# Kernel optimization log

Hardware: AMD Instinct MI355X
Metric: run time of the kernel (lower is better)

The kernel has to match this reference:

```python
import jax, jax.numpy as jnp
import numpy as np
from math import sqrt

N_HEADS = 4
IN_FEATURES = 64
KQ = 64
HEAD_V = IN_FEATURES // N_HEADS  # 16


def setup_inputs() -> dict:
    key = jax.random.key(0)
    ks = jax.random.split(key, 7)
    s = 0.05
    x = jax.random.normal(ks[0], (8192, IN_FEATURES), dtype=jnp.float32)
    # Per-head Linear weights stacked on a leading head axis.
    # torch Linear: y = x @ W.T + b; we store W already transposed: [H, F, E]
    Wq = jax.random.normal(ks[1], (N_HEADS, IN_FEATURES, KQ), dtype=jnp.float32) * s
    bq = jax.random.normal(ks[2], (N_HEADS, KQ), dtype=jnp.float32) * s
    Wk = jax.random.normal(ks[3], (N_HEADS, IN_FEATURES, KQ), dtype=jnp.float32) * s
    bk = jax.random.normal(ks[4], (N_HEADS, KQ), dtype=jnp.float32) * s
    Wv = jax.random.normal(ks[5], (N_HEADS, IN_FEATURES, HEAD_V), dtype=jnp.float32) * s
    bv = jax.random.normal(ks[6], (N_HEADS, HEAD_V), dtype=jnp.float32) * s
    return {"x": x, "Wq": Wq, "bq": bq, "Wk": Wk, "bk": bk, "Wv": Wv, "bv": bv}


def reference(x, Wq, bq, Wk, bk, Wv, bv):
    N, F = x.shape
    scale = 1.0 / sqrt(F)  # original divides by sqrt(in_features), NOT sqrt(kq)
    # Batched-head projections: [H, N, E]
    Q = jnp.einsum('nf,hfe->hne', x, Wq) + bq[:, None, :]
    K = jnp.einsum('nf,hfe->hne', x, Wk) + bk[:, None, :]
    V = jnp.einsum('nf,hfd->hnd', x, Wv) + bv[:, None, :]
    logits = jnp.einsum('hne,hme->hnm', Q, K) * scale  # [H, N, N]
    attn = jax.nn.softmax(logits, axis=-1)
    out_heads = jnp.einsum('hnm,hmd->hnd', attn, V)    # [H, N, HEAD_V]
    # Head i writes columns [i*HEAD_V:(i+1)*HEAD_V] of the output.
    out = jnp.transpose(out_heads, (1, 0, 2)).reshape(N, F)
    return out
```

## Files before the change

### kernel.cpp

```cpp
#include <hip/hip_runtime.h>

typedef __attribute__((ext_vector_type(4))) float f32x4;
typedef __attribute__((ext_vector_type(8))) short bf16x8;
typedef __attribute__((ext_vector_type(4))) short bf16x4;
typedef long fp8x8;

#define NH 4

static __device__ __forceinline__ unsigned short f2bf(float f){
  unsigned u = __float_as_uint(f);
  u += 0x7FFFu + ((u >> 16) & 1u);
  return (unsigned short)(u >> 16);
}

static __device__ __forceinline__ unsigned pack2bf(float a, float b){
  return __builtin_amdgcn_perm(__float_as_uint(b) + 0x8000u,
                               __float_as_uint(a) + 0x8000u, 0x07060302u);
}

static __device__ __forceinline__ unsigned pack2bf_t(float a, float b){
  return __builtin_amdgcn_perm(__float_as_uint(b), __float_as_uint(a), 0x07060302u);
}

static __device__ __forceinline__ int pack_fp8x4(float a, float b, float c, float d){
  int w = __builtin_amdgcn_cvt_pk_fp8_f32(a, b, 0, false);
  w     = __builtin_amdgcn_cvt_pk_fp8_f32(c, d, w, true);
  return w;
}

__global__ __launch_bounds__(256) void wprep_kernel(
    const float* __restrict__ Wq, const float* __restrict__ bq,
    const float* __restrict__ Wk, const float* __restrict__ bk,
    const float* __restrict__ Wv,
    unsigned short* __restrict__ WF, float* __restrict__ bias_s, int n)
{
  __shared__ unsigned short wqT[64*72];
  __shared__ unsigned short wkT[64*72];
  __shared__ unsigned short wvT[16*72];

  const int t = threadIdx.x;
  const int h = blockIdx.x;
  const float S1 = 0.4246609001f;
  const int f = t >> 2, eg = t & 3;

  {
    const float4* g = (const float4*)(Wq + h*4096 + f*64 + eg*16);
    #pragma unroll
    for (int p = 0; p < 4; ++p){
      float4 d = g[p];
      int e0 = eg*16 + p*4;
      wqT[(e0+0)*72 + f] = f2bf(d.x * S1);
      wqT[(e0+1)*72 + f] = f2bf(d.y * S1);
      wqT[(e0+2)*72 + f] = f2bf(d.z * S1);
      wqT[(e0+3)*72 + f] = f2bf(d.w * S1);
    }
  }
  {
    const float4* g = (const float4*)(Wk + h*4096 + f*64 + eg*16);
    #pragma unroll
    for (int p = 0; p < 4; ++p){
      float4 d = g[p];
      int e0 = eg*16 + p*4;
      wkT[(e0+0)*72 + f] = f2bf(d.x * S1);
      wkT[(e0+1)*72 + f] = f2bf(d.y * S1);
      wkT[(e0+2)*72 + f] = f2bf(d.z * S1);
      wkT[(e0+3)*72 + f] = f2bf(d.w * S1);
    }
  }
  {
    float4 d = *(const float4*)(Wv + h*1024 + f*16 + eg*4);
    int d0 = eg*4;
    wvT[(d0+0)*72 + f] = f2bf(d.x);
    wvT[(d0+1)*72 + f] = f2bf(d.y);
    wvT[(d0+2)*72 + f] = f2bf(d.z);
    wvT[(d0+3)*72 + f] = f2bf(d.w);
  }
  if (t < 64)       bias_s[h*128 + t] = bq[h*64 + t] * S1;
  else if (t < 128) bias_s[h*128 + t] = bk[h*64 + (t-64)] * S1;
  __syncthreads();

  const int lane = t & 63, w = t >> 6;
  const int quad = lane >> 4, l16 = lane & 15;
  for (int s = w; s < 18; s += 4){
    const unsigned short* src;
    if (s < 8){      int et = s>>1,     ks = s&1;     src = wqT + (et*16+l16)*72 + ks*32 + quad*8; }
    else if (s < 16){int ft = (s-8)>>1, ks = (s-8)&1; src = wkT + (ft*16+l16)*72 + ks*32 + quad*8; }
    else {           int ks = s-16;                   src = wvT + l16*72 + ks*32 + quad*8; }
    uint4 v = *(const uint4*)src;
    *(uint4*)(WF + ((size_t)(h*18 + s)*64 + lane)*8) = v;
  }
}

__global__ __launch_bounds__(256) void proj_kernel(
    const float* __restrict__ x, const float* __restrict__ bv,
    const unsigned short* __restrict__ WF, const float* __restrict__ bias_s,
    unsigned char* __restrict__ Qfr, unsigned char* __restrict__ Kt,
    unsigned short* __restrict__ Vt, int n)
{
  __shared__ unsigned short xf[8*64*8];
  __shared__ float bql[64], bkl[64], bvl[16];

  const int t  = threadIdx.x;
  const int h  = blockIdx.y;
  const int r0 = blockIdx.x * 64;

  {
    const int r = t >> 2, cg4 = t & 3;
    const float4* g = (const float4*)(x + (size_t)(r0 + r)*64 + cg4*16);
    float4 a = g[0], b = g[1], c = g[2], d = g[3];
    unsigned u0 = pack2bf(a.x,a.y), u1 = pack2bf(a.z,a.w);
    unsigned u2 = pack2bf(b.x,b.y), u3 = pack2bf(b.z,b.w);
    unsigned u4 = pack2bf(c.x,c.y), u5 = pack2bf(c.z,c.w);
    unsigned u6 = pack2bf(d.x,d.y), u7 = pack2bf(d.z,d.w);
    const int it = r >> 4, l16r = r & 15, ks = cg4 >> 1, q0 = (cg4 & 1)*2;
    uint4* dst0 = (uint4*)(xf + ((it*2+ks)*64 + q0*16     + l16r)*8);
    uint4* dst1 = (uint4*)(xf + ((it*2+ks)*64 + (q0+1)*16 + l16r)*8);
    *dst0 = make_uint4(u0,u1,u2,u3);
    *dst1 = make_uint4(u4,u5,u6,u7);
  }
  if (t < 64)        bql[t]     = bias_s[h*128 + t];
  else if (t < 128)  bkl[t-64]  = bias_s[h*128 + t];
  else if (t < 144)  bvl[t-128] = bv[h*16 + (t-128)];
  __syncthreads();

  const int lane = t & 63, w = t >> 6;
  const int quad = lane >> 4, l16 = lane & 15;

  bf16x8 xa[8];
  #pragma unroll
  for (int i = 0; i < 8; ++i)
    xa[i] = *(const bf16x8*)(xf + (i*64 + lane)*8);

  const unsigned short* WFh = WF + (size_t)h*18*64*8;
  bf16x8 wq0 = *(const bf16x8*)(WFh + ((size_t)(     w*2 + 0)*64 + lane)*8);
  bf16x8 wq1 = *(const bf16x8*)(WFh + ((size_t)(     w*2 + 1)*64 + lane)*8);
  bf16x8 wk0 = *(const bf16x8*)(WFh + ((size_t)(8  + w*2 + 0)*64 + lane)*8);
  bf16x8 wk1 = *(const bf16x8*)(WFh + ((size_t)(8  + w*2 + 1)*64 + lane)*8);
  bf16x8 wv0 = *(const bf16x8*)(WFh + ((size_t)16*64 + lane)*8);
  bf16x8 wv1 = *(const bf16x8*)(WFh + ((size_t)17*64 + lane)*8);

  const f32x4 z = {0.f,0.f,0.f,0.f};
  f32x4 accQ[4] = {z,z,z,z};
  f32x4 accK[4] = {z,z,z,z};
  f32x4 accV = z;

  #pragma unroll
  for (int it = 0; it < 4; ++it){
    accQ[it] = __builtin_amdgcn_mfma_f32_16x16x32_bf16(wq0, xa[it*2+0], accQ[it], 0,0,0);
    accQ[it] = __builtin_amdgcn_mfma_f32_16x16x32_bf16(wq1, xa[it*2+1], accQ[it], 0,0,0);
  }
  #pragma unroll
  for (int tt = 0; tt < 4; ++tt){
    accK[tt] = __builtin_amdgcn_mfma_f32_16x16x32_bf16(wk0, xa[tt*2+0], accK[tt], 0,0,0);
    accK[tt] = __builtin_amdgcn_mfma_f32_16x16x32_bf16(wk1, xa[tt*2+1], accK[tt], 0,0,0);
  }
  accV = __builtin_amdgcn_mfma_f32_16x16x32_bf16(xa[w*2+0], wv0, accV, 0,0,0);
  accV = __builtin_amdgcn_mfma_f32_16x16x32_bf16(xa[w*2+1], wv1, accV, 0,0,0);

  {
    const int e0 = w*16 + quad*4;
    const float b0 = bql[e0], b1 = bql[e0+1], b2 = bql[e0+2], b3 = bql[e0+3];
    const int qk = (e0 & 31) >> 3, hf = e0 >> 5, boff = (quad & 1) * 4;
    #pragma unroll
    for (int it = 0; it < 4; ++it){
      unsigned o = pack_fp8x4(accQ[it][0]+b0, accQ[it][1]+b1,
                              accQ[it][2]+b2, accQ[it][3]+b3);
      const int T = (r0 >> 4) + it;
      *(unsigned*)(Qfr + (size_t)h*((size_t)n<<6) + (size_t)T*1024
                       + (qk*16 + l16)*16 + hf*8 + boff) = o;
    }
  }
  {
    const int f0 = w*16 + quad*4;
    const float bk0 = bkl[f0], bk1 = bkl[f0+1], bk2 = bkl[f0+2], bk3 = bkl[f0+3];
    const int qk = (f0 & 31) >> 3, hf = f0 >> 5, boff = (quad & 1) * 4;
    #pragma unroll
    for (int tt = 0; tt < 4; ++tt){
      unsigned o = pack_fp8x4(accK[tt][0]+bk0, accK[tt][1]+bk1,
                              accK[tt][2]+bk2, accK[tt][3]+bk3);
      const int T = (r0 >> 4) + tt;
      *(unsigned*)(Kt + (size_t)h*((size_t)n<<6) + (size_t)T*1024
                      + (qk*16 + l16)*16 + hf*8 + boff) = o;
    }
  }
  {
    float bvv = bvl[l16];
    unsigned v01 = pack2bf(accV[0]+bvv, accV[1]+bvv);
    unsigned v23 = pack2bf(accV[2]+bvv, accV[3]+bvv);
    const int T = (r0 >> 4) + w;
    *(uint2*)(Vt + (size_t)h*((size_t)n<<4)
                 + ((size_t)(T>>1)*64 + lane)*8 + (T&1)*4) = make_uint2(v01, v23);
  }
}

__global__ __launch_bounds__(512, 4) void attn_kernel(
    const unsigned char* __restrict__ Qfr, const unsigned char* __restrict__ Kt,
    const unsigned short* __restrict__ Vt, float* __restrict__ out, int n)
{
  __shared__ float part[7][64][17];

  const int tid  = threadIdx.x;
  const int lane = tid & 63;
  const int jq   = tid >> 6;
  const int bid  = blockIdx.x;
  const int h    = bid & 3;
  const int iblk = bid >> 2;
  const int l16  = lane & 15, quad = lane >> 4;
  const int i0   = iblk*32;
  const int ntq  = (n >> 3) >> 4;
  const int nch  = ntq >> 1;
  const int tile0 = jq * ntq;

  const unsigned char* qfh = Qfr + (size_t)h*((size_t)n<<6);
  longlong2 q0 = *(const longlong2*)(qfh + (size_t)((i0>>4)    )*1024 + lane*16);
  longlong2 q1 = *(const longlong2*)(qfh + (size_t)((i0>>4) + 1)*1024 + lane*16);
  const fp8x8 qf00 = (fp8x8)q0.x;
  const fp8x8 qf01 = (fp8x8)q0.y;
  const fp8x8 qf10 = (fp8x8)q1.x;
  const fp8x8 qf11 = (fp8x8)q1.y;

  const longlong2* ktl = (const longlong2*)(Kt + (size_t)h*((size_t)n<<6)) + (size_t)tile0*64 + lane;
  const uint4*     vtu = (const uint4*)(Vt + (size_t)h*((size_t)n<<4)) + (size_t)(tile0>>1)*64 + lane;

  f32x4 o0  = {0.f,0.f,0.f,0.f};
  f32x4 o1  = {0.f,0.f,0.f,0.f};
  f32x4 la0 = {0.f,0.f,0.f,0.f};
  f32x4 la1 = {0.f,0.f,0.f,0.f};
  const f32x4 z = {0.f,0.f,0.f,0.f};
  const bf16x8 vones = {(short)0x3F80, (short)0x3F80, (short)0x3F80, (short)0x3F80,
                        (short)0x3F80, (short)0x3F80, (short)0x3F80, (short)0x3F80};

  longlong2 ka0 = ktl[0],   ka1 = ktl[64];
  uint4     va  = vtu[0];
  longlong2 kb0 = ktl[128], kb1 = ktl[192];
  uint4     vb  = vtu[64];

#define ATTN_CHUNK(KA, KB, VV)                                                \
  {                                                                           \
    fp8x8 a0 = (fp8x8)KA.x;                                                   \
    fp8x8 a1 = (fp8x8)KA.y;                                                   \
    fp8x8 b0 = (fp8x8)KB.x;                                                   \
    fp8x8 b1 = (fp8x8)KB.y;                                                   \
    f32x4 s0 = __builtin_amdgcn_mfma_f32_16x16x32_fp8_fp8(a0, qf00, z, 0,0,0);\
    s0 = __builtin_amdgcn_mfma_f32_16x16x32_fp8_fp8(a1, qf01, s0, 0,0,0);     \
    f32x4 s1 = __builtin_amdgcn_mfma_f32_16x16x32_fp8_fp8(a0, qf10, z, 0,0,0);\
    s1 = __builtin_amdgcn_mfma_f32_16x16x32_fp8_fp8(a1, qf11, s1, 0,0,0);     \
    f32x4 t0 = __builtin_amdgcn_mfma_f32_16x16x32_fp8_fp8(b0, qf00, z, 0,0,0);\
    t0 = __builtin_amdgcn_mfma_f32_16x16x32_fp8_fp8(b1, qf01, t0, 0,0,0);     \
    f32x4 t1 = __builtin_amdgcn_mfma_f32_16x16x32_fp8_fp8(b0, qf10, z, 0,0,0);\
    t1 = __builtin_amdgcn_mfma_f32_16x16x32_fp8_fp8(b1, qf11, t1, 0,0,0);     \
    float pa00 = __builtin_amdgcn_exp2f(s0[0]);                               \
    float pa01 = __builtin_amdgcn_exp2f(s0[1]);                               \
    float pa02 = __builtin_amdgcn_exp2f(s0[2]);                               \
    float pa03 = __builtin_amdgcn_exp2f(s0[3]);                               \
    float pa10 = __builtin_amdgcn_exp2f(s1[0]);                               \
    float pa11 = __builtin_amdgcn_exp2f(s1[1]);                               \
    float pa12 = __builtin_amdgcn_exp2f(s1[2]);                               \
    float pa13 = __builtin_amdgcn_exp2f(s1[3]);                               \
    float pb00 = __builtin_amdgcn_exp2f(t0[0]);                               \
    float pb01 = __builtin_amdgcn_exp2f(t0[1]);                               \
    float pb02 = __builtin_amdgcn_exp2f(t0[2]);                               \
    float pb03 = __builtin_amdgcn_exp2f(t0[3]);                               \
    float pb10 = __builtin_amdgcn_exp2f(t1[0]);                               \
    float pb11 = __builtin_amdgcn_exp2f(t1[1]);                               \
    float pb12 = __builtin_amdgcn_exp2f(t1[2]);                               \
    float pb13 = __builtin_amdgcn_exp2f(t1[3]);                               \
    union { uint4 u; bf16x8 v; } pq0, pq1, vfu;                               \
    pq0.u = make_uint4(pack2bf_t(pa00,pa01), pack2bf_t(pa02,pa03),            \
                       pack2bf_t(pb00,pb01), pack2bf_t(pb02,pb03));           \
    pq1.u = make_uint4(pack2bf_t(pa10,pa11), pack2bf_t(pa12,pa13),            \
                       pack2bf_t(pb10,pb11), pack2bf_t(pb12,pb13));           \
    vfu.u = VV;                                                               \
    o0  = __builtin_amdgcn_mfma_f32_16x16x32_bf16(pq0.v, vfu.v, o0,  0,0,0);  \
    o1  = __builtin_amdgcn_mfma_f32_16x16x32_bf16(pq1.v, vfu.v, o1,  0,0,0);  \
    la0 = __builtin_amdgcn_mfma_f32_16x16x32_bf16(pq0.v, vones, la0, 0,0,0);  \
    la1 = __builtin_amdgcn_mfma_f32_16x16x32_bf16(pq1.v, vones, la1, 0,0,0);  \
  }

  for (int c = 0; c < nch - 2; c += 2){
    ATTN_CHUNK(ka0, ka1, va)
    ka0 = ktl[256]; ka1 = ktl[320]; va = vtu[128];
    ATTN_CHUNK(kb0, kb1, vb)
    kb0 = ktl[384]; kb1 = ktl[448]; vb = vtu[192];
    ktl += 256; vtu += 128;
  }
  ATTN_CHUNK(ka0, ka1, va)
  ATTN_CHUNK(kb0, kb1, vb)
#undef ATTN_CHUNK

  if (jq > 0){
    float* p = &part[jq-1][lane][0];
    p[ 0]=o0[0];  p[ 1]=o0[1];  p[ 2]=o0[2];  p[ 3]=o0[3];
    p[ 4]=o1[0];  p[ 5]=o1[1];  p[ 6]=o1[2];  p[ 7]=o1[3];
    p[ 8]=la0[0]; p[ 9]=la0[1]; p[10]=la0[2]; p[11]=la0[3];
    p[12]=la1[0]; p[13]=la1[1]; p[14]=la1[2]; p[15]=la1[3];
  }
  __syncthreads();

  if (jq == 0){
    #pragma unroll
    for (int q = 0; q < 7; ++q){
      const float* r = &part[q][lane][0];
      o0[0] +=r[0];  o0[1] +=r[1];  o0[2] +=r[2];  o0[3] +=r[3];
      o1[0] +=r[4];  o1[1] +=r[5];  o1[2] +=r[6];  o1[3] +=r[7];
      la0[0]+=r[8];  la0[1]+=r[9];  la0[2]+=r[10]; la0[3]+=r[11];
      la1[0]+=r[12]; la1[1]+=r[13]; la1[2]+=r[14]; la1[3]+=r[15];
    }
    #pragma unroll
    for (int reg = 0; reg < 4; ++reg){
      int i = quad*4 + reg;
      out[(size_t)(i0 + i)*64      + h*16 + l16] = o0[reg] / la0[reg];
      out[(size_t)(i0 + 16 + i)*64 + h*16 + l16] = o1[reg] / la1[reg];
    }
  }
}

extern "C" void kernel_launch(void* const* d_in, const int* in_sizes, int n_in,
                              void* d_out, int out_size, void* d_ws, size_t ws_size,
                              hipStream_t stream) {
  const float* x  = (const float*)d_in[0];
  const float* Wq = (const float*)d_in[1];
  const float* bq = (const float*)d_in[2];
  const float* Wk = (const float*)d_in[3];
  const float* bk = (const float*)d_in[4];
  const float* Wv = (const float*)d_in[5];
  const float* bv = (const float*)d_in[6];
  float* out = (float*)d_out;

  const int n = in_sizes[0] / 64;

  unsigned char* Qfr  = (unsigned char*)d_ws;
  unsigned char* Kt   = Qfr + (size_t)NH*n*64;
  unsigned short* Vt  = (unsigned short*)(Kt + (size_t)NH*n*64);
  unsigned short* WF  = Vt + (size_t)NH*n*16;
  float* bias_s       = (float*)(WF + (size_t)NH*18*64*8);

  wprep_kernel<<<NH, 256, 0, stream>>>(Wq, bq, Wk, bk, Wv, WF, bias_s, n);
  proj_kernel<<<dim3(n/64, NH), 256, 0, stream>>>(x, bv, WF, bias_s, Qfr, Kt, Vt, n);
  attn_kernel<<<dim3((n/32)*NH), 512, 0, stream>>>(Qfr, Kt, Vt, out, n);
}
```

Measured before the change: 118.0 us.

## Process 64 query rows per attention block to reuse K/V tiles

```diff
diff --git a/kernel.cpp b/kernel.cpp
--- a/kernel.cpp
+++ b/kernel.cpp
@@ -197,7 +197,7 @@
     const unsigned char* __restrict__ Qfr, const unsigned char* __restrict__ Kt,
     const unsigned short* __restrict__ Vt, float* __restrict__ out, int n)
 {
-  __shared__ float part[7][64][17];
+  __shared__ float part[7][64][33];
 
   const int tid  = threadIdx.x;
   const int lane = tid & 63;
@@ -206,7 +206,7 @@
   const int h    = bid & 3;
   const int iblk = bid >> 2;
   const int l16  = lane & 15, quad = lane >> 4;
-  const int i0   = iblk*32;
+  const int i0   = iblk*64;
   const int ntq  = (n >> 3) >> 4;
   const int nch  = ntq >> 1;
   const int tile0 = jq * ntq;
@@ -214,19 +214,19 @@
   const unsigned char* qfh = Qfr + (size_t)h*((size_t)n<<6);
   longlong2 q0 = *(const longlong2*)(qfh + (size_t)((i0>>4)    )*1024 + lane*16);
   longlong2 q1 = *(const longlong2*)(qfh + (size_t)((i0>>4) + 1)*1024 + lane*16);
-  const fp8x8 qf00 = (fp8x8)q0.x;
-  const fp8x8 qf01 = (fp8x8)q0.y;
-  const fp8x8 qf10 = (fp8x8)q1.x;
-  const fp8x8 qf11 = (fp8x8)q1.y;
+  longlong2 q2 = *(const longlong2*)(qfh + (size_t)((i0>>4) + 2)*1024 + lane*16);
+  longlong2 q3 = *(const longlong2*)(qfh + (size_t)((i0>>4) + 3)*1024 + lane*16);
+  const fp8x8 qf00 = (fp8x8)q0.x, qf01 = (fp8x8)q0.y;
+  const fp8x8 qf10 = (fp8x8)q1.x, qf11 = (fp8x8)q1.y;
+  const fp8x8 qf20 = (fp8x8)q2.x, qf21 = (fp8x8)q2.y;
+  const fp8x8 qf30 = (fp8x8)q3.x, qf31 = (fp8x8)q3.y;
 
   const longlong2* ktl = (const longlong2*)(Kt + (size_t)h*((size_t)n<<6)) + (size_t)tile0*64 + lane;
   const uint4*     vtu = (const uint4*)(Vt + (size_t)h*((size_t)n<<4)) + (size_t)(tile0>>1)*64 + lane;
 
-  f32x4 o0  = {0.f,0.f,0.f,0.f};
-  f32x4 o1  = {0.f,0.f,0.f,0.f};
-  f32x4 la0 = {0.f,0.f,0.f,0.f};
-  f32x4 la1 = {0.f,0.f,0.f,0.f};
   const f32x4 z = {0.f,0.f,0.f,0.f};
+  f32x4 o0 = z, o1 = z, o2 = z, o3 = z;
+  f32x4 la0 = z, la1 = z, la2 = z, la3 = z;
   const bf16x8 vones = {(short)0x3F80, (short)0x3F80, (short)0x3F80, (short)0x3F80,
                         (short)0x3F80, (short)0x3F80, (short)0x3F80, (short)0x3F80};
 
@@ -235,46 +235,37 @@
   longlong2 kb0 = ktl[128], kb1 = ktl[192];
   uint4     vb  = vtu[64];
 
+#define ITILE(QA, QB, OO, LL)                                                 \
+  {                                                                           \
+    f32x4 s = __builtin_amdgcn_mfma_f32_16x16x32_fp8_fp8(a0, QA, z, 0,0,0);   \
+    s = __builtin_amdgcn_mfma_f32_16x16x32_fp8_fp8(a1, QB, s, 0,0,0);         \
+    f32x4 u = __builtin_amdgcn_mfma_f32_16x16x32_fp8_fp8(b0, QA, z, 0,0,0);   \
+    u = __builtin_amdgcn_mfma_f32_16x16x32_fp8_fp8(b1, QB, u, 0,0,0);         \
+    float e0 = __builtin_amdgcn_exp2f(s[0]);                                  \
+    float e1 = __builtin_amdgcn_exp2f(s[1]);                                  \
+    float e2 = __builtin_amdgcn_exp2f(s[2]);                                  \
+    float e3 = __builtin_amdgcn_exp2f(s[3]);                                  \
+    float f0 = __builtin_amdgcn_exp2f(u[0]);                                  \
+    float f1 = __builtin_amdgcn_exp2f(u[1]);                                  \
+    float f2 = __builtin_amdgcn_exp2f(u[2]);                                  \
+    float f3 = __builtin_amdgcn_exp2f(u[3]);                                  \
+    union { uint4 uu; bf16x8 v; } pq;                                         \
+    pq.uu = make_uint4(pack2bf_t(e0,e1), pack2bf_t(e2,e3),                    \
+                       pack2bf_t(f0,f1), pack2bf_t(f2,f3));                   \
+    OO = __builtin_amdgcn_mfma_f32_16x16x32_bf16(pq.v, vfv,   OO, 0,0,0);     \
+    LL = __builtin_amdgcn_mfma_f32_16x16x32_bf16(pq.v, vones, LL, 0,0,0);     \
+  }
+
 #define ATTN_CHUNK(KA, KB, VV)                                                \
   {                                                                           \
-    fp8x8 a0 = (fp8x8)KA.x;                                                   \
-    fp8x8 a1 = (fp8x8)KA.y;                                                   \
-    fp8x8 b0 = (fp8x8)KB.x;                                                   \
-    fp8x8 b1 = (fp8x8)KB.y;                                                   \
-    f32x4 s0 = __builtin_amdgcn_mfma_f32_16x16x32_fp8_fp8(a0, qf00, z, 0,0,0);\
-    s0 = __builtin_amdgcn_mfma_f32_16x16x32_fp8_fp8(a1, qf01, s0, 0,0,0);     \
-    f32x4 s1 = __builtin_amdgcn_mfma_f32_16x16x32_fp8_fp8(a0, qf10, z, 0,0,0);\
-    s1 = __builtin_amdgcn_mfma_f32_16x16x32_fp8_fp8(a1, qf11, s1, 0,0,0);     \
-    f32x4 t0 = __builtin_amdgcn_mfma_f32_16x16x32_fp8_fp8(b0, qf00, z, 0,0,0);\
-    t0 = __builtin_amdgcn_mfma_f32_16x16x32_fp8_fp8(b1, qf01, t0, 0,0,0);     \
-    f32x4 t1 = __builtin_amdgcn_mfma_f32_16x16x32_fp8_fp8(b0, qf10, z, 0,0,0);\
-    t1 = __builtin_amdgcn_mfma_f32_16x16x32_fp8_fp8(b1, qf11, t1, 0,0,0);     \
-    float pa00 = __builtin_amdgcn_exp2f(s0[0]);                               \
-    float pa01 = __builtin_amdgcn_exp2f(s0[1]);                               \
-    float pa02 = __builtin_amdgcn_exp2f(s0[2]);                               \
-    float pa03 = __builtin_amdgcn_exp2f(s0[3]);                               \
-    float pa10 = __builtin_amdgcn_exp2f(s1[0]);                               \
-    float pa11 = __builtin_amdgcn_exp2f(s1[1]);                               \
-    float pa12 = __builtin_amdgcn_exp2f(s1[2]);                               \
-    float pa13 = __builtin_amdgcn_exp2f(s1[3]);                               \
-    float pb00 = __builtin_amdgcn_exp2f(t0[0]);                               \
-    float pb01 = __builtin_amdgcn_exp2f(t0[1]);                               \
-    float pb02 = __builtin_amdgcn_exp2f(t0[2]);                               \
-    float pb03 = __builtin_amdgcn_exp2f(t0[3]);                               \
-    float pb10 = __builtin_amdgcn_exp2f(t1[0]);                               \
-    float pb11 = __builtin_amdgcn_exp2f(t1[1]);                               \
-    float pb12 = __builtin_amdgcn_exp2f(t1[2]);                               \
-    float pb13 = __builtin_amdgcn_exp2f(t1[3]);                               \
-    union { uint4 u; bf16x8 v; } pq0, pq1, vfu;                               \
-    pq0.u = make_uint4(pack2bf_t(pa00,pa01), pack2bf_t(pa02,pa03),            \
-                       pack2bf_t(pb00,pb01), pack2bf_t(pb02,pb03));           \
-    pq1.u = make_uint4(pack2bf_t(pa10,pa11), pack2bf_t(pa12,pa13),            \
-                       pack2bf_t(pb10,pb11), pack2bf_t(pb12,pb13));           \
-    vfu.u = VV;                                                               \
-    o0  = __builtin_amdgcn_mfma_f32_16x16x32_bf16(pq0.v, vfu.v, o0,  0,0,0);  \
-    o1  = __builtin_amdgcn_mfma_f32_16x16x32_bf16(pq1.v, vfu.v, o1,  0,0,0);  \
-    la0 = __builtin_amdgcn_mfma_f32_16x16x32_bf16(pq0.v, vones, la0, 0,0,0);  \
-    la1 = __builtin_amdgcn_mfma_f32_16x16x32_bf16(pq1.v, vones, la1, 0,0,0);  \
+    const fp8x8 a0 = (fp8x8)KA.x, a1 = (fp8x8)KA.y;                           \
+    const fp8x8 b0 = (fp8x8)KB.x, b1 = (fp8x8)KB.y;                           \
+    union { uint4 uu; bf16x8 v; } vfu; vfu.uu = VV;                           \
+    const bf16x8 vfv = vfu.v;                                                 \
+    ITILE(qf00, qf01, o0, la0)                                                \
+    ITILE(qf10, qf11, o1, la1)                                                \
+    ITILE(qf20, qf21, o2, la2)                                                \
+    ITILE(qf30, qf31, o3, la3)                                                \
   }
 
   for (int c = 0; c < nch - 2; c += 2){
@@ -287,13 +278,18 @@
   ATTN_CHUNK(ka0, ka1, va)
   ATTN_CHUNK(kb0, kb1, vb)
 #undef ATTN_CHUNK
+#undef ITILE
 
   if (jq > 0){
     float* p = &part[jq-1][lane][0];
     p[ 0]=o0[0];  p[ 1]=o0[1];  p[ 2]=o0[2];  p[ 3]=o0[3];
     p[ 4]=o1[0];  p[ 5]=o1[1];  p[ 6]=o1[2];  p[ 7]=o1[3];
-    p[ 8]=la0[0]; p[ 9]=la0[1]; p[10]=la0[2]; p[11]=la0[3];
-    p[12]=la1[0]; p[13]=la1[1]; p[14]=la1[2]; p[15]=la1[3];
+    p[ 8]=o2[0];  p[ 9]=o2[1];  p[10]=o2[2];  p[11]=o2[3];
+    p[12]=o3[0];  p[13]=o3[1];  p[14]=o3[2];  p[15]=o3[3];
+    p[16]=la0[0]; p[17]=la0[1]; p[18]=la0[2]; p[19]=la0[3];
+    p[20]=la1[0]; p[21]=la1[1]; p[22]=la1[2]; p[23]=la1[3];
+    p[24]=la2[0]; p[25]=la2[1]; p[26]=la2[2]; p[27]=la2[3];
+    p[28]=la3[0]; p[29]=la3[1]; p[30]=la3[2]; p[31]=la3[3];
   }
   __syncthreads();
 
@@ -303,14 +299,20 @@
       const float* r = &part[q][lane][0];
       o0[0] +=r[0];  o0[1] +=r[1];  o0[2] +=r[2];  o0[3] +=r[3];
       o1[0] +=r[4];  o1[1] +=r[5];  o1[2] +=r[6];  o1[3] +=r[7];
-      la0[0]+=r[8];  la0[1]+=r[9];  la0[2]+=r[10]; la0[3]+=r[11];
-      la1[0]+=r[12]; la1[1]+=r[13]; la1[2]+=r[14]; la1[3]+=r[15];
+      o2[0] +=r[8];  o2[1] +=r[9];  o2[2] +=r[10]; o2[3] +=r[11];
+      o3[0] +=r[12]; o3[1] +=r[13]; o3[2] +=r[14]; o3[3] +=r[15];
+      la0[0]+=r[16]; la0[1]+=r[17]; la0[2]+=r[18]; la0[3]+=r[19];
+      la1[0]+=r[20]; la1[1]+=r[21]; la1[2]+=r[22]; la1[3]+=r[23];
+      la2[0]+=r[24]; la2[1]+=r[25]; la2[2]+=r[26]; la2[3]+=r[27];
+      la3[0]+=r[28]; la3[1]+=r[29]; la3[2]+=r[30]; la3[3]+=r[31];
     }
     #pragma unroll
     for (int reg = 0; reg < 4; ++reg){
       int i = quad*4 + reg;
-      out[(size_t)(i0 + i)*64      + h*16 + l16] = o0[reg] / la0[reg];
+      out[(size_t)(i0 +      i)*64 + h*16 + l16] = o0[reg] / la0[reg];
       out[(size_t)(i0 + 16 + i)*64 + h*16 + l16] = o1[reg] / la1[reg];
+      out[(size_t)(i0 + 32 + i)*64 + h*16 + l16] = o2[reg] / la2[reg];
+      out[(size_t)(i0 + 48 + i)*64 + h*16 + l16] = o3[reg] / la3[reg];
     }
   }
 }
@@ -337,5 +339,5 @@
 
   wprep_kernel<<<NH, 256, 0, stream>>>(Wq, bq, Wk, bk, Wv, WF, bias_s, n);
   proj_kernel<<<dim3(n/64, NH), 256, 0, stream>>>(x, bv, WF, bias_s, Qfr, Kt, Vt, n);
-  attn_kernel<<<dim3((n/32)*NH), 512, 0, stream>>>(Qfr, Kt, Vt, out, n);
-}
+  attn_kernel<<<dim3((n/64)*NH), 512, 0, stream>>>(Qfr, Kt, Vt, out, n);
+}
```

New measurement: 117.6 us. Within noise of the previous version (-0.4%).
